# Kernel optimization log

Hardware: AMD Instinct MI355X
Metric: run time of the kernel (lower is better)

## Reference

```python
import jax, jax.numpy as jnp
import numpy as np

N_BINS = 15
DELTA = 1.0 / N_BINS


def setup_inputs() -> dict:
    key = jax.random.key(0)
    k1, k2 = jax.random.split(key)
    N, C = 4_000_000, 10
    # scale 5 -> confident softmax -> low collision entropy so bins [0,1) are populated
    logits = jax.random.normal(k1, (N, C), dtype=jnp.float32) * 5.0
    labels = jax.random.randint(k2, (N,), 0, C)
    return {"logits": logits, "labels": labels}


def reference(logits, labels):
    # probs: [N, C]
    probs = jax.nn.softmax(logits, axis=-1)
    # collision entropy H2 per sample: [N]
    u = -jnp.log2(jnp.sum(probs * probs, axis=-1) + 1e-12)
    err_real = (jnp.argmax(probs, axis=-1) != labels).astype(jnp.float32)  # [N]

    n = u.shape[0]
    # bin b covers [b*DELTA, (b+1)*DELTA); samples with u outside [0,1) go to overflow bin
    bin_idx = jnp.floor(u / DELTA).astype(jnp.int32)
    valid = (u >= 0.0) & (u < 1.0)
    seg = jnp.where(valid, bin_idx, N_BINS)

    vf = valid.astype(jnp.float32)
    counts = jax.ops.segment_sum(vf, seg, num_segments=N_BINS + 1)[:N_BINS]
    sum_u = jax.ops.segment_sum(jnp.where(valid, u, 0.0), seg, num_segments=N_BINS + 1)[:N_BINS]
    sum_err = jax.ops.segment_sum(jnp.where(valid, err_real, 0.0), seg, num_segments=N_BINS + 1)[:N_BINS]

    pi = counts / n                      # population weight per bin
    nonempty = counts > 0
    cnt = jnp.where(nonempty, counts, 1.0)
    u_b = sum_u / cnt                    # mean H2 in bin
    err_b = sum_err / cnt                # empirical error rate in bin

    # risk-from-H2 reference curve
    inner = jnp.clip(2.0 * jnp.exp2(-u_b) - 1.0, 0.0, None)
    r_ref = 0.5 * (1.0 - jnp.sqrt(inner))

    gaps = jnp.where(nonempty, jnp.abs(err_b - r_ref) * pi, 0.0)
    return jnp.sum(gaps)
```

## Files before the change

kernel.cpp:

```cpp
#include <hip/hip_runtime.h>
#include <math.h>

#define NB 15


__global__ __launch_bounds__(256, 4) void bin_kernel(
    const float* __restrict__ logits,
    const int* __restrict__ labels,
    float* __restrict__ acc,
    int N, int numTiles)
{
    __shared__ float4 lds4[2][640];
    __shared__ float s_acc[3 * NB];

    const int t = threadIdx.x;
    if (t < 3 * NB) s_acc[t] = 0.0f;

    int   pk[NB];
    float su[NB];
#pragma unroll
    for (int b = 0; b < NB; ++b) { pk[b] = 0; su[b] = 0.0f; }

    const float4* __restrict__ srcF4 = (const float4*)logits;
    const long long totF4 = (((long long)N * 10) + 3) >> 2;
    float* ldsf = (float*)lds4;

    int tile = blockIdx.x;
    int labCur = 0;

    {
        long long base = (long long)tile * 640;
#pragma unroll
        for (int k = 0; k < 3; ++k) {
            int li = t + (k << 8);
            if (li < 640) {
                long long gi = base + li;
                float4 v = make_float4(0.f, 0.f, 0.f, 0.f);
                if (gi < totF4) v = srcF4[gi];
                lds4[0][li] = v;
            }
        }
        int row = tile * 256 + t;
        labCur = (row < N) ? labels[row] : 0;
    }
    __syncthreads();

    int cur = 0;
    while (tile < numTiles) {
        const int nxt = tile + gridDim.x;
        const bool hasNext = (nxt < numTiles);

        float4 v0, v1, v2;
        int labNext = 0;
        if (hasNext) {
            long long base = (long long)nxt * 640;
            {
                long long gi = base + t;
                v0 = (gi < totF4) ? srcF4[gi] : make_float4(0.f,0.f,0.f,0.f);
            }
            {
                long long gi = base + t + 256;
                v1 = (gi < totF4) ? srcF4[gi] : make_float4(0.f,0.f,0.f,0.f);
            }
            if (t < 128) {
                long long gi = base + t + 512;
                v2 = (gi < totF4) ? srcF4[gi] : make_float4(0.f,0.f,0.f,0.f);
            }
            int row = nxt * 256 + t;
            labNext = (row < N) ? labels[row] : 0;
        }

        {
            const float* r = ldsf + cur * 2560 + t * 10;
            const float2* r2 = (const float2*)r;
            float lv[10];
#pragma unroll
            for (int j = 0; j < 5; ++j) {
                float2 w = r2[j];
                lv[2 * j]     = w.x;
                lv[2 * j + 1] = w.y;
            }
            float m = lv[0];
#pragma unroll
            for (int j = 1; j < 10; ++j) m = fmaxf(m, lv[j]);

            const float c = 1.44269504088896340736f;
            float mc = m * c;
            float Z = 0.0f, S = 0.0f;
#pragma unroll
            for (int j = 0; j < 10; ++j) {
                float e = exp2f(fmaf(lv[j], c, -mc));
                Z += e;
                S = fmaf(e, e, S);
            }
            float ratio = S * __builtin_amdgcn_rcpf(Z * Z);
            float u = -log2f(ratio + 1e-12f);

            int row = tile * 256 + t;
            bool valid = (row < N) & (u >= 0.0f) & (u < 1.0f);
            int bin = -1;
            if (valid) {
                bin = (int)(u * 15.0f);
                if (bin > 14) bin = 14;
            }
            float lvl = r[labCur];
            int e10 = (lvl != m) ? 1 : 0;
            float uu = valid ? u : 0.0f;
            int inc = 1 + (e10 << 16);
#pragma unroll
            for (int b = 0; b < NB; ++b) {
                bool mt = (bin == b);
                pk[b] += mt ? inc : 0;
                su[b] += mt ? uu : 0.0f;
            }
        }

        if (hasNext) {
            lds4[cur ^ 1][t]       = v0;
            lds4[cur ^ 1][t + 256] = v1;
            if (t < 128) lds4[cur ^ 1][t + 512] = v2;
        }
        __syncthreads();
        cur ^= 1;
        tile = nxt;
        labCur = labNext;
    }

    const int lane = t & 63;
#pragma unroll
    for (int b = 0; b < NB; ++b) {
        int   p = pk[b];
        float s = su[b];
#pragma unroll
        for (int off = 1; off < 64; off <<= 1) {
            p += __shfl_xor(p, off, 64);
            s += __shfl_xor(s, off, 64);
        }
        if (lane == 0) {
            atomicAdd(&s_acc[b],          (float)(p & 0xFFFF));
            atomicAdd(&s_acc[NB + b],     s);
            atomicAdd(&s_acc[2 * NB + b], (float)(p >> 16));
        }
    }
    __syncthreads();
    if (t < 3 * NB) {
        float v = s_acc[t];
        if (v != 0.0f) atomicAdd(&acc[t], v);
    }
}

__global__ void finalize_kernel(const float* __restrict__ acc,
                                float* __restrict__ out, float n)
{
    int b = threadIdx.x;
    float gap = 0.0f;
    if (b < NB) {
        float cnt = acc[b];
        if (cnt > 0.0f) {
            float u_b   = acc[NB + b] / cnt;
            float err_b = acc[2 * NB + b] / cnt;
            float inner = 2.0f * exp2f(-u_b) - 1.0f;
            if (inner < 0.0f) inner = 0.0f;
            float r_ref = 0.5f * (1.0f - sqrtf(inner));
            gap = fabsf(err_b - r_ref) * (cnt / n);
        }
    }
#pragma unroll
    for (int off = 32; off >= 1; off >>= 1)
        gap += __shfl_xor(gap, off, 64);
    if (b == 0) out[0] = gap;
}

extern "C" void kernel_launch(void* const* d_in, const int* in_sizes, int n_in,
                              void* d_out, int out_size, void* d_ws, size_t ws_size,
                              hipStream_t stream)
{
    const float* logits = (const float*)d_in[0];
    const int*   labels = (const int*)d_in[1];
    const int N = in_sizes[1];

    float* acc = (float*)d_ws;
    hipMemsetAsync(acc, 0, 3 * NB * sizeof(float), stream);

    const int numTiles = (N + 255) / 256;
    int blocks = numTiles < 1024 ? numTiles : 1024;
    bin_kernel<<<blocks, 256, 0, stream>>>(logits, labels, acc, N, numTiles);
    finalize_kernel<<<1, 64, 0, stream>>>(acc, (float*)d_out, (float)N);
}
```

Before: 248.6 us.

## Replace LDS double-buffered tile staging with direct per-thread loads, two rows per iteration

Drops the shared-memory double buffer and its barriers. Each thread now reads its own 10-float row straight from global memory as float2 loads and processes two rows per iteration for more memory-level parallelism. The label logit is picked with a register select chain instead of an LDS index, and the grid doubles to 2048 blocks. The risk is that per-thread 40-byte strided float2 loads coalesce worse than the earlier contiguous float4 tile loads.

```diff
diff --git a/kernel.cpp b/kernel.cpp
--- a/kernel.cpp
+++ b/kernel.cpp
@@ -4,15 +4,46 @@
 #define NB 15
 
 
+__device__ __forceinline__ void row_stats(const float lv[10], int lab, int N_ok,
+                                          int& bin, float& u, int& e10)
+{
+    float m = lv[0];
+#pragma unroll
+    for (int j = 1; j < 10; ++j) m = fmaxf(m, lv[j]);
+
+    const float c = 1.44269504088896340736f;
+    float mc = m * c;
+    float Z = 0.0f, S = 0.0f;
+#pragma unroll
+    for (int j = 0; j < 10; ++j) {
+        float e = exp2f(fmaf(lv[j], c, -mc));
+        Z += e;
+        S = fmaf(e, e, S);
+    }
+    float ratio = S * __builtin_amdgcn_rcpf(Z * Z);
+    u = -log2f(ratio + 1e-12f);
+
+    bool valid = N_ok && (u >= 0.0f) && (u < 1.0f);
+    bin = -1;
+    if (valid) {
+        bin = (int)(u * 15.0f);
+        if (bin > 14) bin = 14;
+    }
+    if (!valid) u = 0.0f;
+
+    float lvl = lv[0];
+#pragma unroll
+    for (int j = 1; j < 10; ++j) lvl = (lab == j) ? lv[j] : lvl;
+    e10 = (lvl != m) ? 1 : 0;
+}
+
 __global__ __launch_bounds__(256, 4) void bin_kernel(
     const float* __restrict__ logits,
     const int* __restrict__ labels,
     float* __restrict__ acc,
-    int N, int numTiles)
+    int N)
 {
-    __shared__ float4 lds4[2][640];
     __shared__ float s_acc[3 * NB];
-
     const int t = threadIdx.x;
     if (t < 3 * NB) s_acc[t] = 0.0f;
 
@@ -21,109 +52,56 @@
 #pragma unroll
     for (int b = 0; b < NB; ++b) { pk[b] = 0; su[b] = 0.0f; }
 
-    const float4* __restrict__ srcF4 = (const float4*)logits;
-    const long long totF4 = (((long long)N * 10) + 3) >> 2;
-    float* ldsf = (float*)lds4;
+    const float2* __restrict__ src2 = (const float2*)logits;
+    const int stride = gridDim.x * 256;
+    int r = blockIdx.x * 256 + t;
 
-    int tile = blockIdx.x;
-    int labCur = 0;
+    for (; r + stride < N; r += 2 * stride) {
+        const int r2i = r + stride;
+        float a[10], b2[10];
+        {
+            const float2* p = src2 + (long long)r * 5;
+#pragma unroll
+            for (int j = 0; j < 5; ++j) { float2 w = p[j]; a[2*j] = w.x; a[2*j+1] = w.y; }
+        }
+        {
+            const float2* p = src2 + (long long)r2i * 5;
+#pragma unroll
+            for (int j = 0; j < 5; ++j) { float2 w = p[j]; b2[2*j] = w.x; b2[2*j+1] = w.y; }
+        }
+        int labA = labels[r];
+        int labB = labels[r2i];
 
-    {
-        long long base = (long long)tile * 640;
+        int binA, eA, binB, eB;
+        float uA, uB;
+        row_stats(a,  labA, 1, binA, uA, eA);
+        row_stats(b2, labB, 1, binB, uB, eB);
+
+        int incA = 1 + (eA << 16);
+        int incB = 1 + (eB << 16);
 #pragma unroll
-        for (int k = 0; k < 3; ++k) {
-            int li = t + (k << 8);
-            if (li < 640) {
-                long long gi = base + li;
-                float4 v = make_float4(0.f, 0.f, 0.f, 0.f);
-                if (gi < totF4) v = srcF4[gi];
-                lds4[0][li] = v;
-            }
+        for (int b = 0; b < NB; ++b) {
+            bool mA = (binA == b);
+            bool mB = (binB == b);
+            pk[b] += (mA ? incA : 0) + (mB ? incB : 0);
+            su[b] += (mA ? uA : 0.0f) + (mB ? uB : 0.0f);
         }
-        int row = tile * 256 + t;
-        labCur = (row < N) ? labels[row] : 0;
     }
-    __syncthreads();
-
-    int cur = 0;
-    while (tile < numTiles) {
-        const int nxt = tile + gridDim.x;
-        const bool hasNext = (nxt < numTiles);
-
-        float4 v0, v1, v2;
-        int labNext = 0;
-        if (hasNext) {
-            long long base = (long long)nxt * 640;
-            {
-                long long gi = base + t;
-                v0 = (gi < totF4) ? srcF4[gi] : make_float4(0.f,0.f,0.f,0.f);
-            }
-            {
-                long long gi = base + t + 256;
-                v1 = (gi < totF4) ? srcF4[gi] : make_float4(0.f,0.f,0.f,0.f);
-            }
-            if (t < 128) {
-                long long gi = base + t + 512;
-                v2 = (gi < totF4) ? srcF4[gi] : make_float4(0.f,0.f,0.f,0.f);
-            }
-            int row = nxt * 256 + t;
-            labNext = (row < N) ? labels[row] : 0;
+    if (r < N) {
+        float a[10];
+        const float2* p = src2 + (long long)r * 5;
+#pragma unroll
+        for (int j = 0; j < 5; ++j) { float2 w = p[j]; a[2*j] = w.x; a[2*j+1] = w.y; }
+        int lab = labels[r];
+        int bin, e10; float u;
+        row_stats(a, lab, 1, bin, u, e10);
+        int inc = 1 + (e10 << 16);
+#pragma unroll
+        for (int b = 0; b < NB; ++b) {
+            bool mt = (bin == b);
+            pk[b] += mt ? inc : 0;
+            su[b] += mt ? u : 0.0f;
         }
-
-        {
-            const float* r = ldsf + cur * 2560 + t * 10;
-            const float2* r2 = (const float2*)r;
-            float lv[10];
-#pragma unroll
-            for (int j = 0; j < 5; ++j) {
-                float2 w = r2[j];
-                lv[2 * j]     = w.x;
-                lv[2 * j + 1] = w.y;
-            }
-            float m = lv[0];
-#pragma unroll
-            for (int j = 1; j < 10; ++j) m = fmaxf(m, lv[j]);
-
-            const float c = 1.44269504088896340736f;
-            float mc = m * c;
-            float Z = 0.0f, S = 0.0f;
-#pragma unroll
-            for (int j = 0; j < 10; ++j) {
-                float e = exp2f(fmaf(lv[j], c, -mc));
-                Z += e;
-                S = fmaf(e, e, S);
-            }
-            float ratio = S * __builtin_amdgcn_rcpf(Z * Z);
-            float u = -log2f(ratio + 1e-12f);
-
-            int row = tile * 256 + t;
-            bool valid = (row < N) & (u >= 0.0f) & (u < 1.0f);
-            int bin = -1;
-            if (valid) {
-                bin = (int)(u * 15.0f);
-                if (bin > 14) bin = 14;
-            }
-            float lvl = r[labCur];
-            int e10 = (lvl != m) ? 1 : 0;
-            float uu = valid ? u : 0.0f;
-            int inc = 1 + (e10 << 16);
-#pragma unroll
-            for (int b = 0; b < NB; ++b) {
-                bool mt = (bin == b);
-                pk[b] += mt ? inc : 0;
-                su[b] += mt ? uu : 0.0f;
-            }
-        }
-
-        if (hasNext) {
-            lds4[cur ^ 1][t]       = v0;
-            lds4[cur ^ 1][t + 256] = v1;
-            if (t < 128) lds4[cur ^ 1][t + 512] = v2;
-        }
-        __syncthreads();
-        cur ^= 1;
-        tile = nxt;
-        labCur = labNext;
     }
 
     const int lane = t & 63;
@@ -182,8 +160,9 @@
     float* acc = (float*)d_ws;
     hipMemsetAsync(acc, 0, 3 * NB * sizeof(float), stream);
 
-    const int numTiles = (N + 255) / 256;
-    int blocks = numTiles < 1024 ? numTiles : 1024;
-    bin_kernel<<<blocks, 256, 0, stream>>>(logits, labels, acc, N, numTiles);
+    int blocks = 2048;
+    int maxBlocks = (N + 255) / 256;
+    if (blocks > maxBlocks) blocks = maxBlocks;
+    bin_kernel<<<blocks, 256, 0, stream>>>(logits, labels, acc, N);
     finalize_kernel<<<1, 64, 0, stream>>>(acc, (float*)d_out, (float)N);
 }
```

Measured after the change: 265.0 us. 6.6% more time.

## Pad LDS row stride to avoid bank conflicts and drop double-buffered prefetch

Applied to the files above, without the earlier changes.

Coalesced float4 loads are now scattered into LDS with an odd row stride of 11 floats, so per-row reads no longer hit stride-10 bank conflicts. The explicit double-buffered register prefetch is replaced by a simple single-buffer loop with two barriers per tile. The grid cap rises from 1024 to 2048 blocks and the occupancy hint in launch bounds is dropped. Scalar scatter stores add LDS instructions, and losing the explicit prefetch relies on occupancy to hide memory latency. The row<N check is removed from validity, so padded rows beyond N could land in a bin, though N is a multiple of 256 here.

```diff
diff --git a/kernel.cpp b/kernel.cpp
--- a/kernel.cpp
+++ b/kernel.cpp
@@ -2,15 +2,31 @@
 #include <math.h>
 
 #define NB 15
+#define TROWS 256
+#define TF4   640
+#define LSTRIDE 11
 
 
-__global__ __launch_bounds__(256, 4) void bin_kernel(
+__device__ __forceinline__ void scatter4(float* lds, int li, float4 v)
+{
+    unsigned f   = (unsigned)li * 4u;
+    unsigned row = f / 10u;
+    unsigned off = f - row * 10u;
+    unsigned a0  = row * LSTRIDE + off;
+    lds[a0]     = v.x;
+    lds[a0 + 1] = v.y;
+    unsigned a1 = (off == 8u) ? (a0 + 3u) : (a0 + 2u);
+    lds[a1]     = v.z;
+    lds[a1 + 1] = v.w;
+}
+
+__global__ __launch_bounds__(256) void bin_kernel(
     const float* __restrict__ logits,
     const int* __restrict__ labels,
     float* __restrict__ acc,
     int N, int numTiles)
 {
-    __shared__ float4 lds4[2][640];
+    __shared__ float lds[TROWS * LSTRIDE];
     __shared__ float s_acc[3 * NB];
 
     const int t = threadIdx.x;
@@ -21,109 +37,69 @@
 #pragma unroll
     for (int b = 0; b < NB; ++b) { pk[b] = 0; su[b] = 0.0f; }
 
-    const float4* __restrict__ srcF4 = (const float4*)logits;
-    const long long totF4 = (((long long)N * 10) + 3) >> 2;
-    float* ldsf = (float*)lds4;
+    const float4* __restrict__ src4 = (const float4*)logits;
+    const long long totF4 = ((long long)N * 10) >> 2;
+    const float4 zero4 = make_float4(0.f, 0.f, 0.f, 0.f);
 
-    int tile = blockIdx.x;
-    int labCur = 0;
+    for (int tile = blockIdx.x; tile < numTiles; tile += gridDim.x) {
+        const long long base = (long long)tile * TF4;
+        long long g0 = base + t;
+        long long g1 = base + t + 256;
+        long long g2 = base + t + 512;
+        float4 v0 = (g0 < totF4) ? src4[g0] : zero4;
+        float4 v1 = (g1 < totF4) ? src4[g1] : zero4;
+        float4 v2 = zero4;
+        const bool has2 = (t < TF4 - 512);
+        if (has2 && g2 < totF4) v2 = src4[g2];
 
-    {
-        long long base = (long long)tile * 640;
+        const int gr  = tile * TROWS + t;
+        const int lab = (gr < N) ? labels[gr] : 0;
+
+        __syncthreads();
+        scatter4(lds, t,       v0);
+        scatter4(lds, t + 256, v1);
+        if (has2) scatter4(lds, t + 512, v2);
+        __syncthreads();
+
+        const float* r = lds + t * LSTRIDE;
+        float lv[10];
 #pragma unroll
-        for (int k = 0; k < 3; ++k) {
-            int li = t + (k << 8);
-            if (li < 640) {
-                long long gi = base + li;
-                float4 v = make_float4(0.f, 0.f, 0.f, 0.f);
-                if (gi < totF4) v = srcF4[gi];
-                lds4[0][li] = v;
-            }
+        for (int j = 0; j < 10; ++j) lv[j] = r[j];
+
+        float m = lv[0];
+#pragma unroll
+        for (int j = 1; j < 10; ++j) m = fmaxf(m, lv[j]);
+
+        const float c = 1.44269504088896340736f;
+        float mc = m * c;
+        float Z = 0.0f, S = 0.0f;
+#pragma unroll
+        for (int j = 0; j < 10; ++j) {
+            float e = exp2f(fmaf(lv[j], c, -mc));
+            Z += e;
+            S = fmaf(e, e, S);
         }
-        int row = tile * 256 + t;
-        labCur = (row < N) ? labels[row] : 0;
-    }
-    __syncthreads();
+        float ratio = S * __builtin_amdgcn_rcpf(Z * Z);
+        float u = -log2f(ratio + 1e-12f);
 
-    int cur = 0;
-    while (tile < numTiles) {
-        const int nxt = tile + gridDim.x;
-        const bool hasNext = (nxt < numTiles);
+        bool valid = (u >= 0.0f) && (u < 1.0f);
+        int bin = -1;
+        if (valid) {
+            bin = (int)(u * 15.0f);
+            if (bin > 14) bin = 14;
+        }
+        float uu = valid ? u : 0.0f;
 
-        float4 v0, v1, v2;
-        int labNext = 0;
-        if (hasNext) {
-            long long base = (long long)nxt * 640;
-            {
-                long long gi = base + t;
-                v0 = (gi < totF4) ? srcF4[gi] : make_float4(0.f,0.f,0.f,0.f);
-            }
-            {
-                long long gi = base + t + 256;
-                v1 = (gi < totF4) ? srcF4[gi] : make_float4(0.f,0.f,0.f,0.f);
-            }
-            if (t < 128) {
-                long long gi = base + t + 512;
-                v2 = (gi < totF4) ? srcF4[gi] : make_float4(0.f,0.f,0.f,0.f);
-            }
-            int row = nxt * 256 + t;
-            labNext = (row < N) ? labels[row] : 0;
+        float lvl = r[lab];
+        int e10 = (lvl != m) ? 1 : 0;
+        int inc = 1 + (e10 << 16);
+
+#pragma unroll
+        for (int b = 0; b < NB; ++b) {
+            bool mt = (bin == b);
+            pk[b] += mt ? inc : 0;
+            su[b] += mt ? uu : 0.0f;
         }
-
-        {
-            const float* r = ldsf + cur * 2560 + t * 10;
-            const float2* r2 = (const float2*)r;
-            float lv[10];
-#pragma unroll
-            for (int j = 0; j < 5; ++j) {
-                float2 w = r2[j];
-                lv[2 * j]     = w.x;
-                lv[2 * j + 1] = w.y;
-            }
-            float m = lv[0];
-#pragma unroll
-            for (int j = 1; j < 10; ++j) m = fmaxf(m, lv[j]);
-
-            const float c = 1.44269504088896340736f;
-            float mc = m * c;
-            float Z = 0.0f, S = 0.0f;
-#pragma unroll
-            for (int j = 0; j < 10; ++j) {
-                float e = exp2f(fmaf(lv[j], c, -mc));
-                Z += e;
-                S = fmaf(e, e, S);
-            }
-            float ratio = S * __builtin_amdgcn_rcpf(Z * Z);
-            float u = -log2f(ratio + 1e-12f);
-
-            int row = tile * 256 + t;
-            bool valid = (row < N) & (u >= 0.0f) & (u < 1.0f);
-            int bin = -1;
-            if (valid) {
-                bin = (int)(u * 15.0f);
-                if (bin > 14) bin = 14;
-            }
-            float lvl = r[labCur];
-            int e10 = (lvl != m) ? 1 : 0;
-            float uu = valid ? u : 0.0f;
-            int inc = 1 + (e10 << 16);
-#pragma unroll
-            for (int b = 0; b < NB; ++b) {
-                bool mt = (bin == b);
-                pk[b] += mt ? inc : 0;
-                su[b] += mt ? uu : 0.0f;
-            }
-        }
-
-        if (hasNext) {
-            lds4[cur ^ 1][t]       = v0;
-            lds4[cur ^ 1][t + 256] = v1;
-            if (t < 128) lds4[cur ^ 1][t + 512] = v2;
-        }
-        __syncthreads();
-        cur ^= 1;
-        tile = nxt;
-        labCur = labNext;
     }
 
     const int lane = t & 63;
@@ -182,8 +158,8 @@
     float* acc = (float*)d_ws;
     hipMemsetAsync(acc, 0, 3 * NB * sizeof(float), stream);
 
-    const int numTiles = (N + 255) / 256;
-    int blocks = numTiles < 1024 ? numTiles : 1024;
+    const int numTiles = (N + TROWS - 1) / TROWS;
+    int blocks = numTiles < 2048 ? numTiles : 2048;
     bin_kernel<<<blocks, 256, 0, stream>>>(logits, labels, acc, N, numTiles);
     finalize_kernel<<<1, 64, 0, stream>>>(acc, (float*)d_out, (float)N);
 }
```

New measurement: 251.0 us. No clear change (+1.0%).
